# Kernel optimization log

Hardware: AMD Instinct MI355X
Metric: run time of the kernel (lower is better)

Reference implementation:

```python
import jax, jax.numpy as jnp
import numpy as np
from jax import lax

T, B = 128, 256          # rollout length x num envs
H, W, C = 7, 7, 3        # minigrid obs
HID = 128                # lstm hidden
NA = 7                   # actions
NFLAT = 64 * 4 * 4       # conv flatten (7->6->5->4)


def setup_inputs() -> dict:
    key = jax.random.key(0)
    ks = jax.random.split(key, 20)
    N = T * B
    obs = jax.random.randint(ks[0], (N, H, W, C), 0, 11).astype(jnp.float32)
    done = (jax.random.uniform(ks[1], (N,)) < 0.05).astype(jnp.float32)
    h0 = jnp.zeros((1, B, HID), jnp.float32)
    c0 = jnp.zeros((1, B, HID), jnp.float32)
    s = 0.1
    conv1_w = jax.random.normal(ks[2], (16, C, 2, 2)) * s
    conv1_b = jnp.zeros((16,), jnp.float32)
    conv2_w = jax.random.normal(ks[3], (32, 16, 2, 2)) * s
    conv2_b = jnp.zeros((32,), jnp.float32)
    conv3_w = jax.random.normal(ks[4], (64, 32, 2, 2)) * s
    conv3_b = jnp.zeros((64,), jnp.float32)
    w_ih = jax.random.normal(ks[5], (4 * HID, NFLAT)) * 0.03
    w_hh = jax.random.normal(ks[6], (4 * HID, HID)) * 0.08
    b_ih = jnp.zeros((4 * HID,), jnp.float32)
    b_hh = jnp.zeros((4 * HID,), jnp.float32)
    actor_w = jax.random.normal(ks[7], (NA, HID)) * 0.01
    actor_b = jnp.zeros((NA,), jnp.float32)
    critic_w = jax.random.normal(ks[8], (1, HID)) * 0.08
    critic_b = jnp.zeros((1,), jnp.float32)
    return dict(obs=obs, done=done, h0=h0, c0=c0,
                conv1_w=conv1_w, conv1_b=conv1_b,
                conv2_w=conv2_w, conv2_b=conv2_b,
                conv3_w=conv3_w, conv3_b=conv3_b,
                w_ih=w_ih, w_hh=w_hh, b_ih=b_ih, b_hh=b_hh,
                actor_w=actor_w, actor_b=actor_b,
                critic_w=critic_w, critic_b=critic_b)


def _conv(x, w, b):
    # x: [N, Cin, h, w], w: [Cout, Cin, 2, 2], VALID, stride 1
    y = lax.conv_general_dilated(x, w, (1, 1), 'VALID',
                                 dimension_numbers=('NCHW', 'OIHW', 'NCHW'))
    return jax.nn.relu(y + b[None, :, None, None])


def reference(obs, done, h0, c0,
              conv1_w, conv1_b, conv2_w, conv2_b, conv3_w, conv3_b,
              w_ih, w_hh, b_ih, b_hh, actor_w, actor_b, critic_w, critic_b):
    N = obs.shape[0]
    x = jnp.transpose(obs, (0, 3, 1, 2))            # NHWC -> NCHW
    x = _conv(x, conv1_w, conv1_b)
    x = _conv(x, conv2_w, conv2_b)
    x = _conv(x, conv3_w, conv3_b)
    feat = x.reshape(N, -1)                          # [T*B, 1024]

    nb = h0.shape[1]
    xs = feat.reshape(-1, nb, feat.shape[-1])        # [T, B, 1024]
    ds = done.reshape(-1, nb)                        # [T, B]
    bias = b_ih + b_hh

    def step(carry, inp):
        h, c = carry                                  # [B, HID]
        x_t, d_t = inp
        m = (1.0 - d_t)[:, None]
        h = m * h
        c = m * c
        gates = x_t @ w_ih.T + h @ w_hh.T + bias      # [B, 4*HID]
        i, f, g, o = jnp.split(gates, 4, axis=-1)     # torch gate order i,f,g,o
        i = jax.nn.sigmoid(i)
        f = jax.nn.sigmoid(f)
        g = jnp.tanh(g)
        o = jax.nn.sigmoid(o)
        c = f * c + i * g
        h = o * jnp.tanh(c)
        return (h, c), h

    (hT, cT), hs = lax.scan(step, (h0[0], c0[0]), (xs, ds))
    hid = hs.reshape(N, -1)                           # [T*B, HID]
    logits = hid @ actor_w.T + actor_b                # [T*B, NA]
    value = hid @ critic_w.T + critic_b               # [T*B, 1]
    out = jnp.concatenate([logits, value], axis=-1)   # [T*B, NA+1]
    return out, hT[None], cT[None]
```

## Files before the change

kernel.cpp:

```cpp
#include <hip/hip_runtime.h>
#include <hip/hip_bf16.h>


#define N_IMG   32768
#define T_LEN   128
#define B_ENV   256
#define HID     128

typedef _Float16 f16x8 __attribute__((ext_vector_type(8)));
typedef _Float16 f16x2 __attribute__((ext_vector_type(2)));
typedef float    f32x4 __attribute__((ext_vector_type(4)));
typedef unsigned short ushort8v __attribute__((ext_vector_type(8)));
typedef unsigned short ushort4v __attribute__((ext_vector_type(4)));

#if defined(__has_builtin)
#if __has_builtin(__builtin_amdgcn_exp2f)
#define FEXP2(x) __builtin_amdgcn_exp2f(x)
#endif
#if __has_builtin(__builtin_amdgcn_rcpf)
#define FRCP(x) __builtin_amdgcn_rcpf(x)
#endif
#endif
#ifndef FEXP2
#define FEXP2(x) exp2f(x)
#endif
#ifndef FRCP
#define FRCP(x) (1.0f / (x))
#endif

__device__ __forceinline__ float sigm_(float x) {
    return FRCP(1.0f + FEXP2(-1.44269504f * x));
}
__device__ __forceinline__ float tanh_(float x) {
    return fmaf(-2.0f, FRCP(1.0f + FEXP2(2.88539008f * x)), 1.0f);
}

__device__ __forceinline__ unsigned short f2h(float x) {
    _Float16 h = (_Float16)x;
    union { _Float16 h; unsigned short u; } un; un.h = h;
    return un.u;
}

#if defined(__has_builtin)
#if __has_builtin(__builtin_amdgcn_fdot2)
#define HAVE_FDOT2 1
#endif
#endif

__device__ __forceinline__ float dot2_(f16x2 a, f16x2 b, float c) {
#ifdef HAVE_FDOT2
    return __builtin_amdgcn_fdot2(a, b, c, false);
#else
    c = fmaf((float)a[0], (float)b[0], c);
    return fmaf((float)a[1], (float)b[1], c);
#endif
}

#define P0(v) __builtin_shufflevector(v, v, 0, 1)
#define P1(v) __builtin_shufflevector(v, v, 2, 3)
#define P2(v) __builtin_shufflevector(v, v, 4, 5)
#define P3(v) __builtin_shufflevector(v, v, 6, 7)

__device__ __forceinline__ float bfly_sum4(float x) {
    int y = __builtin_amdgcn_update_dpp(0, __float_as_int(x), 0xB1, 0xF, 0xF, true);
    x += __int_as_float(y);
    y = __builtin_amdgcn_update_dpp(0, __float_as_int(x), 0x4E, 0xF, 0xF, true);
    return x + __int_as_float(y);
}

#define GLDS16(g, l) __builtin_amdgcn_global_load_lds( \
    (const __attribute__((address_space(1))) unsigned int*)(g), \
    (__attribute__((address_space(3))) unsigned int*)(l), 16, 0, 0)

__global__ void prep_all(const float* __restrict__ w_ih, unsigned short* __restrict__ wb,
                         const float* __restrict__ w2, const float* __restrict__ w3,
                         unsigned short* __restrict__ wb2g, unsigned short* __restrict__ wb3g,
                         const float* __restrict__ w_hh, unsigned short* __restrict__ whhr)
{
    const int bid = blockIdx.x, tid = threadIdx.x;
    if (bid < 2048) {
        const int idx = bid * 256 + tid;
        const int np = idx >> 10, kk = idx & 1023;
        const int p = kk >> 6, co = kk & 63;
        const int g = np & 3, ci = np >> 2;
        wb[idx] = f2h(w_ih[(g * 128 + ci) * 1024 + co * 16 + p]);
    } else if (bid < 2088) {
        const int t = (bid - 2048) * 256 + tid;
        if (t < 2048) {
            const int j = t & 7, lane = (t >> 3) & 63, f = t >> 9;
            const int ky = f >> 1, ct = f & 1;
            const int k = ((lane >> 4) << 3) + j, kx = k >> 4, ci = k & 15;
            wb2g[t] = f2h(w2[(ct * 16 + (lane & 15)) * 64 + ci * 4 + ky * 2 + kx]);
        } else {
            const int u = t - 2048;
            const int j = u & 7, lane = (u >> 3) & 63, f = u >> 9;
            const int ct = f >> 2, pos = f & 3;
            const int ci = ((lane >> 4) << 3) + j;
            wb3g[u] = f2h(w3[(ct * 16 + (lane & 15)) * 128 + ci * 4 + pos]);
        }
    } else {
        const int idx = (bid - 2088) * 256 + tid;
        const int thr = idx >> 7, r = idx & 127;
        const int g = r >> 5, k = r & 31;
        const int ci = thr >> 2, s = thr & 3;
        whhr[idx] = f2h(w_hh[(g * 128 + ci) * 128 + s * 32 + k]);
    }
}

__global__ __launch_bounds__(256, 2) void conv_fused(
    const float* __restrict__ obs,
    const float* __restrict__ w1, const float* __restrict__ b1,
    const float* __restrict__ b2, const float* __restrict__ b3,
    const unsigned short* __restrict__ wb2g,
    const unsigned short* __restrict__ wb3g,
    unsigned short* __restrict__ featb)
{
    __shared__ __align__(16) unsigned char u1[25856];
    __shared__ __align__(16) unsigned char u2[33024];
    __shared__ float w1s[192];
    __shared__ float b1s[16];

    float* s_obs = (float*)u1;
    unsigned short* c2s = (unsigned short*)u1;
    unsigned short* c1s = (unsigned short*)u2;
    unsigned short* c3s = (unsigned short*)u2;

    const int tid = threadIdx.x, lane = tid & 63, wv = tid >> 6;
    const int base = blockIdx.x * 16;

    if (tid < 192) w1s[tid] = w1[tid];
    if (tid < 16)  b1s[tid] = b1[tid];
    for (int i = tid; i < 16 * 147; i += 256) {
        const int im = i / 147, r = i - im * 147;
        s_obs[im * 148 + r] = obs[(size_t)(base + im) * 147 + r];
    }
    __syncthreads();

    {
        const int img = tid & 15;
        const float* ob = &s_obs[img * 148];
        for (int p = tid >> 4; p < 36; p += 16) {
            const int py = p / 6, px = p % 6;
            float o[12];
#pragma unroll
            for (int ky = 0; ky < 2; ky++)
#pragma unroll
                for (int kx = 0; kx < 2; kx++)
#pragma unroll
                    for (int cc = 0; cc < 3; cc++)
                        o[cc * 4 + ky * 2 + kx] = ob[((py + ky) * 7 + px + kx) * 3 + cc];
            unsigned short res[16];
#pragma unroll
            for (int ci = 0; ci < 16; ci++) {
                float a = b1s[ci];
#pragma unroll
                for (int q = 0; q < 12; q++) a = fmaf(o[q], w1s[ci * 12 + q], a);
                res[ci] = f2h(fmaxf(a, 0.0f));
            }
            *(ushort8v*)&c1s[img * 584 + p * 16]     = *(ushort8v*)&res[0];
            *(ushort8v*)&c1s[img * 584 + p * 16 + 8] = *(ushort8v*)&res[8];
        }
    }
    __syncthreads();

    {
        const int ct = wv & 1, par = wv >> 1;
        const int img = lane & 15, kq = lane >> 4;
        f16x8 wA[2];
        wA[0] = *(const f16x8*)&wb2g[(0 + ct) * 512 + lane * 8];
        wA[1] = *(const f16x8*)&wb2g[(2 + ct) * 512 + lane * 8];
        const float4 b2v = *(const float4*)&b2[ct * 16 + kq * 4];
#pragma unroll 2
        for (int p = par; p < 25; p += 2) {
            const int py = p / 5, px = p % 5;
            f32x4 acc = {0.f, 0.f, 0.f, 0.f};
#pragma unroll
            for (int ky = 0; ky < 2; ky++) {
                const int pix = (py + ky) * 6 + px + (kq >> 1);
                const f16x8 bv = *(const f16x8*)&c1s[img * 584 + pix * 16 + (kq & 1) * 8];
                acc = __builtin_amdgcn_mfma_f32_16x16x32_f16(wA[ky], bv, acc, 0, 0, 0);
            }
            unsigned short r4[4];
            r4[0] = f2h(fmaxf(acc[0] + b2v.x, 0.0f));
            r4[1] = f2h(fmaxf(acc[1] + b2v.y, 0.0f));
            r4[2] = f2h(fmaxf(acc[2] + b2v.z, 0.0f));
            r4[3] = f2h(fmaxf(acc[3] + b2v.w, 0.0f));
            *(ushort4v*)&c2s[img * 808 + p * 32 + ct * 16 + kq * 4] = *(ushort4v*)&r4[0];
        }
    }
    __syncthreads();

    {
        const int ct = wv;
        const int img = lane & 15, kq = lane >> 4;
        f16x8 wA3[4];
#pragma unroll
        for (int pos = 0; pos < 4; pos++)
            wA3[pos] = *(const f16x8*)&wb3g[(ct * 4 + pos) * 512 + lane * 8];
        const float4 b3v = *(const float4*)&b3[ct * 16 + kq * 4];
#pragma unroll 4
        for (int p = 0; p < 16; p++) {
            const int py = p >> 2, px = p & 3;
            f32x4 acc = {0.f, 0.f, 0.f, 0.f};
#pragma unroll
            for (int pos = 0; pos < 4; pos++) {
                const int pix = (py + (pos >> 1)) * 5 + px + (pos & 1);
                const f16x8 bv = *(const f16x8*)&c2s[img * 808 + pix * 32 + kq * 8];
                acc = __builtin_amdgcn_mfma_f32_16x16x32_f16(wA3[pos], bv, acc, 0, 0, 0);
            }
            unsigned short r4[4];
            r4[0] = f2h(fmaxf(acc[0] + b3v.x, 0.0f));
            r4[1] = f2h(fmaxf(acc[1] + b3v.y, 0.0f));
            r4[2] = f2h(fmaxf(acc[2] + b3v.z, 0.0f));
            r4[3] = f2h(fmaxf(acc[3] + b3v.w, 0.0f));
            *(ushort4v*)&c3s[img * 1032 + p * 64 + ct * 16 + kq * 4] = *(ushort4v*)&r4[0];
        }
    }
    __syncthreads();

#pragma unroll
    for (int i = 0; i < 8; i++) {
        const int gi = i * 2048 + tid * 8;
        const int img = gi >> 10, flat = gi & 1023;
        *(ushort8v*)&featb[(size_t)(base + img) * 1024 + flat] =
            *(const ushort8v*)&c3s[img * 1032 + flat];
    }
}

__global__ __launch_bounds__(256, 2) void gemm_xproj_mfma(
    const unsigned short* __restrict__ A,
    const unsigned short* __restrict__ W,
    float* __restrict__ C)
{
    __shared__ unsigned short As[2][128 * 32];
    __shared__ unsigned short Bs[2][128 * 32];

    const int tid  = threadIdx.x;
    const int bx = blockIdx.x & 3;
    const int by = blockIdx.x >> 2;
    const int m0 = by * 128, n0 = bx * 128;
    const int lane = tid & 63, wave = tid >> 6;
    const int wm = (wave >> 1) * 64, wn = (wave & 1) * 64;
    const int srow = tid >> 2, sseg = tid & 3;

    const unsigned short* Ag = A + (size_t)(m0 + srow) * 1024 + sseg * 8;
    const unsigned short* Wg = W + (size_t)(n0 + srow) * 1024 + sseg * 8;

    f32x4 acc[4][4];
#pragma unroll
    for (int i = 0; i < 4; i++)
#pragma unroll
        for (int j = 0; j < 4; j++) acc[i][j] = (f32x4){0.f, 0.f, 0.f, 0.f};

    const int fr = lane & 15, fq = lane >> 4;

#define STAGEK(bb, k0) do {                                                \
        GLDS16(Ag + (k0),             (char*)&As[bb][0] + tid * 16);       \
        GLDS16(Ag + (k0) + 64 * 1024, (char*)&As[bb][0] + tid * 16 + 4096);\
        GLDS16(Wg + (k0),             (char*)&Bs[bb][0] + tid * 16);       \
        GLDS16(Wg + (k0) + 64 * 1024, (char*)&Bs[bb][0] + tid * 16 + 4096);\
    } while (0)

    STAGEK(0, 0);
    asm volatile("s_waitcnt vmcnt(0)" ::: "memory");
    __syncthreads();

    int cur = 0;
    for (int ks = 0; ks < 32; ks++) {
        if (ks + 1 < 32) STAGEK(cur ^ 1, (ks + 1) * 32);

        f16x8 af[4], bfv[4];
#pragma unroll
        for (int i = 0; i < 4; i++)
            af[i] = *(const f16x8*)&As[cur][(wm + i * 16 + fr) * 32 + fq * 8];
#pragma unroll
        for (int j = 0; j < 4; j++)
            bfv[j] = *(const f16x8*)&Bs[cur][(wn + j * 16 + fr) * 32 + fq * 8];
#pragma unroll
        for (int i = 0; i < 4; i++)
#pragma unroll
            for (int j = 0; j < 4; j++)
                acc[i][j] = __builtin_amdgcn_mfma_f32_16x16x32_f16(af[i], bfv[j], acc[i][j], 0, 0, 0);

        asm volatile("s_waitcnt vmcnt(0)" ::: "memory");
        __syncthreads();
        cur ^= 1;
    }
#undef STAGEK

    const int cr = fq * 4, cc = fr;
#pragma unroll
    for (int i = 0; i < 4; i++) {
#pragma unroll
        for (int j = 0; j < 4; j++) {
            float* cp = &C[(size_t)(m0 + wm + i * 16 + cr) * 512 + (n0 + wn + j * 16 + cc)];
#pragma unroll
            for (int r = 0; r < 4; r++)
                cp[(size_t)r * 512] = acc[i][j][r];
        }
    }
}

__global__ __launch_bounds__(512) __attribute__((amdgpu_waves_per_eu(2, 2)))
void lstm_bfly(
    const float* __restrict__ xproj, const float* __restrict__ done,
    const float* __restrict__ h0, const float* __restrict__ c0,
    const unsigned short* __restrict__ whhr,
    const float* __restrict__ b_ih, const float* __restrict__ b_hh,
    unsigned short* __restrict__ hid16, float* __restrict__ out)
{
    const int b   = blockIdx.x;
    const int tid = threadIdx.x;
    const int ci  = tid >> 2;
    const int s   = tid & 3;

    __shared__ __align__(16) _Float16 hbuf[2][HID];

    f16x8 w[4][4];
    {
        const unsigned short* wp = whhr + (size_t)tid * 128;
#pragma unroll
        for (int g = 0; g < 4; g++)
#pragma unroll
            for (int i = 0; i < 4; i++)
                w[g][i] = *(const f16x8*)&wp[g * 32 + i * 8];
    }
    const float bias_l = b_ih[s * 128 + ci] + b_hh[s * 128 + ci];

    float c = c0[b * HID + ci];
    float h = h0[b * HID + ci];
    float dcur = done[b];

    if (tid < HID)
        hbuf[0][tid] = (_Float16)(h0[b * HID + tid] * (1.0f - dcur));

    float xq = bias_l + xproj[(size_t)b * 512 + ci * 4 + s];
    __syncthreads();

#define DOTBLK(i, c0_, c1_, c2_, c3_)                                           \
    {                                                                           \
        const f16x8 hv8 = *(const f16x8*)&hbuf[p][s * 32 + (i) * 8];            \
        const f16x2 hp0 = P0(hv8), hp1 = P1(hv8), hp2 = P2(hv8), hp3 = P3(hv8); \
        c0_ = dot2_(P0(w[0][i]), hp0, c0_); c0_ = dot2_(P1(w[0][i]), hp1, c0_); \
        c0_ = dot2_(P2(w[0][i]), hp2, c0_); c0_ = dot2_(P3(w[0][i]), hp3, c0_); \
        c1_ = dot2_(P0(w[1][i]), hp0, c1_); c1_ = dot2_(P1(w[1][i]), hp1, c1_); \
        c1_ = dot2_(P2(w[1][i]), hp2, c1_); c1_ = dot2_(P3(w[1][i]), hp3, c1_); \
        c2_ = dot2_(P0(w[2][i]), hp0, c2_); c2_ = dot2_(P1(w[2][i]), hp1, c2_); \
        c2_ = dot2_(P2(w[2][i]), hp2, c2_); c2_ = dot2_(P3(w[2][i]), hp3, c2_); \
        c3_ = dot2_(P0(w[3][i]), hp0, c3_); c3_ = dot2_(P1(w[3][i]), hp1, c3_); \
        c3_ = dot2_(P2(w[3][i]), hp2, c3_); c3_ = dot2_(P3(w[3][i]), hp3, c3_); \
    }

    int p = 0;
    for (int t = 0; t < T_LEN; t++) {
        const int tn = (t + 1 < T_LEN) ? t + 1 : t;
        const float xqn = bias_l + xproj[((size_t)tn * B_ENV + b) * 512 + ci * 4 + s];
        const float dnn = done[tn * B_ENV + b];

        float a0 = (s == 0) ? xq : 0.0f;
        float a1 = (s == 1) ? xq : 0.0f;
        float a2 = (s == 2) ? xq : 0.0f;
        float a3 = (s == 3) ? xq : 0.0f;
        float b0 = 0.f, b1 = 0.f, b2 = 0.f, b3 = 0.f;
        DOTBLK(0, a0, a1, a2, a3)
        DOTBLK(1, b0, b1, b2, b3)
        DOTBLK(2, a0, a1, a2, a3)
        DOTBLK(3, b0, b1, b2, b3)
        a0 += b0; a1 += b1; a2 += b2; a3 += b3;

        a0 = bfly_sum4(a0); a1 = bfly_sum4(a1);
        a2 = bfly_sum4(a2); a3 = bfly_sum4(a3);

        const float gi = sigm_(a0), gf = sigm_(a1);
        const float gg = tanh_(a2), go = sigm_(a3);
        const float m = 1.0f - dcur;
        c = fmaf(gf, c * m, gi * gg);
        h = go * tanh_(c);

        if (s == 0) {
            hid16[((size_t)t * B_ENV + b) * HID + ci] = f2h(h);
            hbuf[p ^ 1][ci] = (_Float16)(h * (1.0f - dnn));
        }

        xq = xqn; dcur = dnn; p ^= 1;
        __syncthreads();
    }

    if (s == 0) {
        out[262144 + b * HID + ci] = h;
        out[294912 + b * HID + ci] = c;
    }
#undef DOTBLK
}

__global__ __launch_bounds__(256, 2) void heads_kernel(
    const unsigned short* __restrict__ hid16,
    const float* __restrict__ aw, const float* __restrict__ ab,
    const float* __restrict__ cw, const float* __restrict__ cb,
    float* __restrict__ out)
{
    __shared__ float hs[32 * 129];
    __shared__ float ws[8 * 130];
    __shared__ float bs[8];

    const int tid = threadIdx.x;
    const int n0 = blockIdx.x * 32;

    for (int i = tid; i < 1024; i += 256) {
        const int r = i >> 7, k = i & 127;
        ws[r * 130 + k] = (r < 7) ? aw[r * 128 + k] : cw[k];
    }
    if (tid < 8) bs[tid] = (tid < 7) ? ab[tid] : cb[0];
    for (int i = tid; i < 512; i += 256) {
        const int r = i >> 4, k8 = (i & 15) * 8;
        const ushort8v v = *(const ushort8v*)&hid16[(size_t)(n0 + r) * 128 + k8];
#pragma unroll
        for (int q = 0; q < 8; q++) {
            union { unsigned short u; _Float16 h; } un; un.u = v[q];
            hs[r * 129 + k8 + q] = (float)un.h;
        }
    }
    __syncthreads();

    const int r = tid >> 3, jj = tid & 7;
    float acc = bs[jj];
    const float* hp = &hs[r * 129];
    const float* wp = &ws[jj * 130];
#pragma unroll
    for (int k = 0; k < 128; k++) acc = fmaf(hp[k], wp[k], acc);
    out[(size_t)(n0 + r) * 8 + jj] = acc;
}

extern "C" void kernel_launch(void* const* d_in, const int* in_sizes, int n_in,
                              void* d_out, int out_size, void* d_ws, size_t ws_size,
                              hipStream_t stream)
{
    (void)in_sizes; (void)n_in; (void)out_size; (void)ws_size;

    const float* obs  = (const float*)d_in[0];
    const float* done = (const float*)d_in[1];
    const float* h0   = (const float*)d_in[2];
    const float* c0   = (const float*)d_in[3];
    const float* w1   = (const float*)d_in[4];
    const float* b1   = (const float*)d_in[5];
    const float* w2   = (const float*)d_in[6];
    const float* b2   = (const float*)d_in[7];
    const float* w3   = (const float*)d_in[8];
    const float* b3   = (const float*)d_in[9];
    const float* w_ih = (const float*)d_in[10];
    const float* w_hh = (const float*)d_in[11];
    const float* b_ih = (const float*)d_in[12];
    const float* b_hh = (const float*)d_in[13];
    const float* aw   = (const float*)d_in[14];
    const float* ab   = (const float*)d_in[15];
    const float* cw   = (const float*)d_in[16];
    const float* cb   = (const float*)d_in[17];
    float* out = (float*)d_out;

    unsigned short* featb = (unsigned short*)d_ws;
    unsigned short* wb    = featb + 33554432ull;
    unsigned short* wb2g  = wb    + 524288ull;
    unsigned short* wb3g  = wb2g  + 2048ull;
    float* xproj = (float*)(wb3g + 8192ull + 2048ull);
    unsigned short* hid16 = (unsigned short*)(xproj + 16777216ull);
    unsigned short* whhr  = hid16 + 4194304ull;

    prep_all<<<2344, 256, 0, stream>>>(w_ih, wb, w2, w3, wb2g, wb3g, w_hh, whhr);
    conv_fused<<<2048, 256, 0, stream>>>(obs, w1, b1, b2, b3, wb2g, wb3g, featb);
    gemm_xproj_mfma<<<1024, 256, 0, stream>>>(featb, wb, xproj);
    lstm_bfly<<<256, 512, 0, stream>>>(xproj, done, h0, c0, whhr, b_ih, b_hh, hid16, out);
    heads_kernel<<<1024, 256, 0, stream>>>(hid16, aw, ab, cw, cb, out);
}
```

Baseline: 281.6 us.

## Split LSTM gate dot products across 8 lanes per hidden unit

After: 306.2 us. 8.7% more time.

```diff
diff --git a/kernel.cpp b/kernel.cpp
--- a/kernel.cpp
+++ b/kernel.cpp
@@ -66,6 +66,10 @@
     x += __int_as_float(y);
     y = __builtin_amdgcn_update_dpp(0, __float_as_int(x), 0x4E, 0xF, 0xF, true);
     return x + __int_as_float(y);
+}
+
+__device__ __forceinline__ float swz_xor4(float x) {
+    return __int_as_float(__builtin_amdgcn_ds_swizzle(__float_as_int(x), 0x101F));
 }
 
 #define GLDS16(g, l) __builtin_amdgcn_global_load_lds( \
@@ -100,10 +104,12 @@
         }
     } else {
         const int idx = (bid - 2088) * 256 + tid;
-        const int thr = idx >> 7, r = idx & 127;
-        const int g = r >> 5, k = r & 31;
-        const int ci = thr >> 2, s = thr & 3;
-        whhr[idx] = f2h(w_hh[(g * 128 + ci) * 128 + s * 32 + k]);
+        const int thr = idx >> 6, r = idx & 63;
+        const int gg = r >> 5, k = r & 31;
+        const int ci = thr >> 3, s = thr & 7;
+        const int kq = s & 3, gp = s >> 2;
+        const int g = gp * 2 + gg;
+        whhr[idx] = f2h(w_hh[(g * 128 + ci) * 128 + kq * 32 + k]);
     }
 }
 
@@ -301,7 +307,7 @@
     }
 }
 
-__global__ __launch_bounds__(512) __attribute__((amdgpu_waves_per_eu(2, 2)))
+__global__ __launch_bounds__(1024) __attribute__((amdgpu_waves_per_eu(4, 4)))
 void lstm_bfly(
     const float* __restrict__ xproj, const float* __restrict__ done,
     const float* __restrict__ h0, const float* __restrict__ c0,
@@ -311,21 +317,26 @@
 {
     const int b   = blockIdx.x;
     const int tid = threadIdx.x;
-    const int ci  = tid >> 2;
-    const int s   = tid & 3;
+    const int ci  = tid >> 3;
+    const int s   = tid & 7;
+    const int kq  = s & 3;
+    const int gp  = s >> 2;
 
     __shared__ __align__(16) _Float16 hbuf[2][HID];
 
-    f16x8 w[4][4];
+    f16x8 w[2][4];
     {
-        const unsigned short* wp = whhr + (size_t)tid * 128;
-#pragma unroll
-        for (int g = 0; g < 4; g++)
+        const unsigned short* wp = whhr + (size_t)tid * 64;
+#pragma unroll
+        for (int gg = 0; gg < 2; gg++)
 #pragma unroll
             for (int i = 0; i < 4; i++)
-                w[g][i] = *(const f16x8*)&wp[g * 32 + i * 8];
-    }
-    const float bias_l = b_ih[s * 128 + ci] + b_hh[s * 128 + ci];
+                w[gg][i] = *(const f16x8*)&wp[gg * 32 + i * 8];
+    }
+    const int gq = 2 * gp + (kq & 1);
+    const float bias_l = b_ih[gq * 128 + ci] + b_hh[gq * 128 + ci];
+    const int xrow = ci * 4 + gq;
+    const bool xact = (kq < 2);
 
     float c = c0[b * HID + ci];
     float h = h0[b * HID + ci];
@@ -334,45 +345,46 @@
     if (tid < HID)
         hbuf[0][tid] = (_Float16)(h0[b * HID + tid] * (1.0f - dcur));
 
-    float xq = bias_l + xproj[(size_t)b * 512 + ci * 4 + s];
-    __syncthreads();
-
-#define DOTBLK(i, c0_, c1_, c2_, c3_)                                           \
+    float xq = bias_l + xproj[(size_t)b * 512 + xrow];
+    __syncthreads();
+
+#define DOTBLK2(i, cA_, cB_)                                                    \
     {                                                                           \
-        const f16x8 hv8 = *(const f16x8*)&hbuf[p][s * 32 + (i) * 8];            \
+        const f16x8 hv8 = *(const f16x8*)&hbuf[p][kq * 32 + (i) * 8];           \
         const f16x2 hp0 = P0(hv8), hp1 = P1(hv8), hp2 = P2(hv8), hp3 = P3(hv8); \
-        c0_ = dot2_(P0(w[0][i]), hp0, c0_); c0_ = dot2_(P1(w[0][i]), hp1, c0_); \
-        c0_ = dot2_(P2(w[0][i]), hp2, c0_); c0_ = dot2_(P3(w[0][i]), hp3, c0_); \
-        c1_ = dot2_(P0(w[1][i]), hp0, c1_); c1_ = dot2_(P1(w[1][i]), hp1, c1_); \
-        c1_ = dot2_(P2(w[1][i]), hp2, c1_); c1_ = dot2_(P3(w[1][i]), hp3, c1_); \
-        c2_ = dot2_(P0(w[2][i]), hp0, c2_); c2_ = dot2_(P1(w[2][i]), hp1, c2_); \
-        c2_ = dot2_(P2(w[2][i]), hp2, c2_); c2_ = dot2_(P3(w[2][i]), hp3, c2_); \
-        c3_ = dot2_(P0(w[3][i]), hp0, c3_); c3_ = dot2_(P1(w[3][i]), hp1, c3_); \
-        c3_ = dot2_(P2(w[3][i]), hp2, c3_); c3_ = dot2_(P3(w[3][i]), hp3, c3_); \
+        cA_ = dot2_(P0(w[0][i]), hp0, cA_); cA_ = dot2_(P1(w[0][i]), hp1, cA_); \
+        cA_ = dot2_(P2(w[0][i]), hp2, cA_); cA_ = dot2_(P3(w[0][i]), hp3, cA_); \
+        cB_ = dot2_(P0(w[1][i]), hp0, cB_); cB_ = dot2_(P1(w[1][i]), hp1, cB_); \
+        cB_ = dot2_(P2(w[1][i]), hp2, cB_); cB_ = dot2_(P3(w[1][i]), hp3, cB_); \
     }
 
     int p = 0;
     for (int t = 0; t < T_LEN; t++) {
         const int tn = (t + 1 < T_LEN) ? t + 1 : t;
-        const float xqn = bias_l + xproj[((size_t)tn * B_ENV + b) * 512 + ci * 4 + s];
+        const float xqn = bias_l + xproj[((size_t)tn * B_ENV + b) * 512 + xrow];
         const float dnn = done[tn * B_ENV + b];
 
-        float a0 = (s == 0) ? xq : 0.0f;
-        float a1 = (s == 1) ? xq : 0.0f;
-        float a2 = (s == 2) ? xq : 0.0f;
-        float a3 = (s == 3) ? xq : 0.0f;
-        float b0 = 0.f, b1 = 0.f, b2 = 0.f, b3 = 0.f;
-        DOTBLK(0, a0, a1, a2, a3)
-        DOTBLK(1, b0, b1, b2, b3)
-        DOTBLK(2, a0, a1, a2, a3)
-        DOTBLK(3, b0, b1, b2, b3)
-        a0 += b0; a1 += b1; a2 += b2; a3 += b3;
-
-        a0 = bfly_sum4(a0); a1 = bfly_sum4(a1);
-        a2 = bfly_sum4(a2); a3 = bfly_sum4(a3);
-
-        const float gi = sigm_(a0), gf = sigm_(a1);
-        const float gg = tanh_(a2), go = sigm_(a3);
+        float aA = (xact && kq == 0) ? xq : 0.0f;
+        float aB = (xact && kq == 1) ? xq : 0.0f;
+        float bA = 0.f, bB = 0.f;
+        DOTBLK2(0, aA, aB)
+        DOTBLK2(1, bA, bB)
+        DOTBLK2(2, aA, aB)
+        DOTBLK2(3, bA, bB)
+        float sA = aA + bA, sB = aB + bB;
+
+        sA = bfly_sum4(sA); sB = bfly_sum4(sB);
+
+        const float oA = swz_xor4(sA);
+        const float oB = swz_xor4(sB);
+
+        const float vi = (gp == 0) ? sA : oA;
+        const float vf = (gp == 0) ? sB : oB;
+        const float vg = (gp == 0) ? oA : sA;
+        const float vo = (gp == 0) ? oB : sB;
+
+        const float gi = sigm_(vi), gf = sigm_(vf);
+        const float gg = tanh_(vg), go = sigm_(vo);
         const float m = 1.0f - dcur;
         c = fmaf(gf, c * m, gi * gg);
         h = go * tanh_(c);
@@ -390,7 +402,7 @@
         out[262144 + b * HID + ci] = h;
         out[294912 + b * HID + ci] = c;
     }
-#undef DOTBLK
+#undef DOTBLK2
 }
 
 __global__ __launch_bounds__(256, 2) void heads_kernel(
@@ -468,6 +480,6 @@
     prep_all<<<2344, 256, 0, stream>>>(w_ih, wb, w2, w3, wb2g, wb3g, w_hh, whhr);
     conv_fused<<<2048, 256, 0, stream>>>(obs, w1, b1, b2, b3, wb2g, wb3g, featb);
     gemm_xproj_mfma<<<1024, 256, 0, stream>>>(featb, wb, xproj);
-    lstm_bfly<<<256, 512, 0, stream>>>(xproj, done, h0, c0, whhr, b_ih, b_hh, hid16, out);
+    lstm_bfly<<<256, 1024, 0, stream>>>(xproj, done, h0, c0, whhr, b_ih, b_hh, hid16, out);
     heads_kernel<<<1024, 256, 0, stream>>>(hid16, aw, ab, cw, cb, out);
 }
```
